# Kernel tuning notes

Hardware: AMD Instinct MI355X
Metric: run time of the kernel (lower is better)

Reference implementation:

```python
import jax, jax.numpy as jnp
import numpy as np

USER_NUM, ITEM_NUM, FACTOR = 138493, 26744, 64
BATCH, N_COLS = 8192, 67  # 1 user + 2 positives + 64 negatives


def setup_inputs() -> dict:
    key = jax.random.key(0)
    k1, k2, k3 = jax.random.split(key, 3)
    one_batch = jax.random.randint(k1, (BATCH, N_COLS), 0, ITEM_NUM, dtype=jnp.int64 if jax.config.jax_enable_x64 else jnp.int32)
    embed_user = jax.random.normal(k2, (USER_NUM, FACTOR), dtype=jnp.float32) * 0.01
    embed_item = jax.random.normal(k3, (ITEM_NUM, FACTOR), dtype=jnp.float32) * 0.01
    return {"one_batch": one_batch, "embed_user": embed_user, "embed_item": embed_item}


def reference(one_batch, embed_user, embed_item):
    user_batch = one_batch[:, 0]          # [B]
    item_batch = one_batch[:, 1:]         # [B, 2+Nneg]
    user_i = embed_user[user_batch]       # [B, D]
    item_i = embed_item[item_batch]       # [B, 2+Nneg, D]

    # scores for the two positives
    z_ai = jnp.einsum('bd,bd->b', user_i, item_i[:, 0, :])
    z_aj = jnp.einsum('bd,bd->b', user_i, item_i[:, 1, :])

    # fun_z with flag=True: |z_ai - z_aj| clamped at 0.5 (pos_sim2 is computed
    # in the original but unused and identical to pos_sim1 by symmetry)
    d = jnp.abs(z_ai - z_aj)
    pos_sim1 = jnp.where(d > 0.5, 0.5, d)

    # all negative scores at once (vectorizes the original Python loop)
    z_ak = jnp.einsum('bd,bnd->bn', user_i, item_i[:, 2:, :])  # [B, Nneg]
    # fun_z with flag=False: -log(sigmoid(z_pos - z_neg))
    neg_sim1 = -jax.nn.log_sigmoid(z_ai[:, None] - z_ak)       # [B, Nneg]
    neg_sim2 = -jax.nn.log_sigmoid(z_aj[:, None] - z_ak)
    one_pn = neg_sim1 + neg_sim2                                # [B, Nneg]

    loss_m6 = one_pn.sum(axis=1)        # running sum over negatives
    loss_m6_min = one_pn.max(axis=1)    # 'min' in the source is actually a running max

    loss_posdis = -jnp.mean(jax.nn.log_sigmoid(pos_sim1 * 2.0 - loss_m6_min))
    loss_pre = loss_posdis + loss_m6.mean()

    l2_regulization = 0.01 * ((user_i ** 2 + (item_i ** 2).sum(axis=1)).sum(axis=-1)).mean()
    loss = loss_pre + l2_regulization
    return (loss, l2_regulization)
```

## Files before the change

### kernel.cpp

```cpp
#include <hip/hip_runtime.h>
#include <math.h>

#define BATCH   8192
#define NCOLS   67
#define DFAC    64
#define THREADS 256
#define WPB     4
#define NBLOCKS (BATCH / WPB)

__device__ __forceinline__ float softplus_f(float t) {
    return fmaxf(t, 0.f) + log1pf(expf(-fabsf(t)));
}
__device__ __forceinline__ float logsig_f(float x) { return -softplus_f(-x); }

__device__ __forceinline__ float wave_sum(float v) {
    #pragma unroll
    for (int off = 32; off; off >>= 1) v += __shfl_xor(v, off);
    return v;
}
__device__ __forceinline__ float wave_max(float v) {
    #pragma unroll
    for (int off = 32; off; off >>= 1) v = fmaxf(v, __shfl_xor(v, off));
    return v;
}

__global__ __launch_bounds__(THREADS) void bpr_main(
    const int*   __restrict__ one_batch,
    const float* __restrict__ eu,
    const float* __restrict__ ei,
    float*       __restrict__ partials)
{
    const int lane = threadIdx.x & 63;
    const int wave = threadIdx.x >> 6;
    const int r    = blockIdx.x * WPB + wave;

    const int rl = lane & 3;
    const int rg = lane >> 2;

    __shared__ float zbuf[WPB][68];

    const int* idx = one_batch + r * NCOLS;

    const int myidx  = idx[lane];
    const int myidx2 = idx[64 + (lane < 3 ? lane : 2)];

    const int uidx = __builtin_amdgcn_readfirstlane(myidx);

    float4 u4[4];
    #pragma unroll
    for (int j = 0; j < 4; ++j)
        u4[j] = *(const float4*)(eu + (size_t)uidx * DFAC + j * 16 + rl * 4);

    float usq = 0.f;
    #pragma unroll
    for (int j = 0; j < 4; ++j)
        usq += u4[j].x*u4[j].x + u4[j].y*u4[j].y + u4[j].z*u4[j].z + u4[j].w*u4[j].w;

    float acc_sq = 0.f;

    #pragma unroll
    for (int s = 0; s < 5; ++s) {
        const int  rr    = s * 16 + rg;
        const bool valid = (rr < 66);
        int col = 1 + rr;
        if (col > 66) col = 66;
        const int ridx = (col < 64) ? __shfl(myidx, col)
                                    : __shfl(myidx2, col - 64);

        const float* vrow = ei + (size_t)ridx * DFAC + rl * 4;
        float pd = 0.f, sq = 0.f;
        #pragma unroll
        for (int j = 0; j < 4; ++j) {
            const float4 v4 = *(const float4*)(vrow + j * 16);
            pd += v4.x*u4[j].x + v4.y*u4[j].y + v4.z*u4[j].z + v4.w*u4[j].w;
            sq += v4.x*v4.x + v4.y*v4.y + v4.z*v4.z + v4.w*v4.w;
        }
        if (valid) acc_sq += sq;

        pd += __shfl_xor(pd, 1);
        pd += __shfl_xor(pd, 2);
        if (valid && rl == 0) zbuf[wave][col] = pd;
    }

    const float z_ai = zbuf[wave][1];
    const float z_aj = zbuf[wave][2];
    const float zak  = zbuf[wave][3 + lane];

    const float one_pn = softplus_f(zak - z_ai) + softplus_f(zak - z_aj);

    const float m6max = wave_max(one_pn);

    float acc_pos = 0.f;
    if (lane == 0) {
        const float dd  = fabsf(z_ai - z_aj);
        const float pos = fminf(dd, 0.5f);
        acc_pos = logsig_f(pos * 2.f - m6max);
    }

    const float acc_m6 = wave_sum(one_pn);
    const float acc_l2 = wave_sum(acc_sq + usq * 0.0625f);

    __shared__ float red[WPB][3];
    if (lane == 0) {
        red[wave][0] = acc_pos;
        red[wave][1] = acc_m6;
        red[wave][2] = acc_l2;
    }
    __syncthreads();
    if (threadIdx.x == 0) {
        float p = 0.f, m = 0.f, l = 0.f;
        #pragma unroll
        for (int w = 0; w < WPB; ++w) {
            p += red[w][0]; m += red[w][1]; l += red[w][2];
        }
        partials[blockIdx.x * 3 + 0] = p;
        partials[blockIdx.x * 3 + 1] = m;
        partials[blockIdx.x * 3 + 2] = l;
    }
}

__global__ __launch_bounds__(256) void bpr_finalize(
    const float* __restrict__ partials, float* __restrict__ out)
{
    float p = 0.f, m = 0.f, l = 0.f;
    for (int i = threadIdx.x; i < NBLOCKS; i += 256) {
        p += partials[i * 3 + 0];
        m += partials[i * 3 + 1];
        l += partials[i * 3 + 2];
    }
    p = wave_sum(p); m = wave_sum(m); l = wave_sum(l);

    __shared__ float red[4][3];
    const int lane = threadIdx.x & 63, wave = threadIdx.x >> 6;
    if (lane == 0) { red[wave][0] = p; red[wave][1] = m; red[wave][2] = l; }
    __syncthreads();
    if (threadIdx.x == 0) {
        #pragma unroll
        for (int w = 1; w < 4; ++w) { p += red[w][0]; m += red[w][1]; l += red[w][2]; }
        const float inv = 1.f / (float)BATCH;
        const float l2   = 0.01f * l * inv;
        const float loss = (-p * inv) + m * inv + l2;
        out[0] = loss;
        out[1] = l2;
    }
}

extern "C" void kernel_launch(void* const* d_in, const int* in_sizes, int n_in,
                              void* d_out, int out_size, void* d_ws, size_t ws_size,
                              hipStream_t stream) {
    const int*   one_batch = (const int*)d_in[0];
    const float* eu        = (const float*)d_in[1];
    const float* ei        = (const float*)d_in[2];
    float* out = (float*)d_out;
    float* partials = (float*)d_ws;

    bpr_main<<<NBLOCKS, THREADS, 0, stream>>>(one_batch, eu, ei, partials);
    bpr_finalize<<<1, 256, 0, stream>>>(partials, out);
}
```

Baseline: 23.55 us.

## Convert item embeddings to bf16 in workspace before gather-dot kernel

Adds a pre-pass kernel that converts the whole item embedding table to bf16 in the workspace on every call. The main kernel then gathers half-size rows, with each lane owning 16 contiguous elements, to cut gather bandwidth. An fp32 fallback path is kept for when the workspace is too small, and invalid rows now skip their loads. The conversion reads and writes the full table (about 6.8 MB) every call, which may cost more than the gather saves, and bf16 rounding reduces accuracy.

```diff
diff --git a/kernel.cpp b/kernel.cpp
--- a/kernel.cpp
+++ b/kernel.cpp
@@ -4,10 +4,15 @@
 #define BATCH   8192
 #define NCOLS   67
 #define DFAC    64
+#define ITEMS   26744
 #define THREADS 256
 #define WPB     4
 #define NBLOCKS (BATCH / WPB)
 
+#define PARTIALS_OFF   0
+#define ITEMBF16_OFF   32768
+#define WS_NEEDED      (ITEMBF16_OFF + (size_t)ITEMS * DFAC * 2)
+
 __device__ __forceinline__ float softplus_f(float t) {
     return fmaxf(t, 0.f) + log1pf(expf(-fabsf(t)));
 }
@@ -24,11 +29,32 @@
     return v;
 }
 
-__global__ __launch_bounds__(THREADS) void bpr_main(
-    const int*   __restrict__ one_batch,
-    const float* __restrict__ eu,
-    const float* __restrict__ ei,
-    float*       __restrict__ partials)
+__device__ __forceinline__ unsigned bf16rne(float f) {
+    unsigned u = __float_as_uint(f);
+    return (u + 0x7FFFu + ((u >> 16) & 1u)) >> 16;
+}
+
+__global__ __launch_bounds__(256) void cvt_items(
+    const float* __restrict__ ei, unsigned* __restrict__ out )
+{
+    const int t = blockIdx.x * 256 + threadIdx.x;
+    const int n8 = ITEMS * DFAC / 8;
+    if (t >= n8) return;
+    const float4 a = *(const float4*)(ei + (size_t)t * 8);
+    const float4 b = *(const float4*)(ei + (size_t)t * 8 + 4);
+    uint4 o;
+    o.x = bf16rne(a.x) | (bf16rne(a.y) << 16);
+    o.y = bf16rne(a.z) | (bf16rne(a.w) << 16);
+    o.z = bf16rne(b.x) | (bf16rne(b.y) << 16);
+    o.w = bf16rne(b.z) | (bf16rne(b.w) << 16);
+    *(uint4*)(out + (size_t)t * 4) = o;
+}
+
+__global__ __launch_bounds__(THREADS) void bpr_main_bf16(
+    const int*      __restrict__ one_batch,
+    const float*    __restrict__ eu,
+    const unsigned* __restrict__ eib,
+    float*          __restrict__ partials)
 {
     const int lane = threadIdx.x & 63;
     const int wave = threadIdx.x >> 6;
@@ -40,16 +66,14 @@
     __shared__ float zbuf[WPB][68];
 
     const int* idx = one_batch + r * NCOLS;
-
     const int myidx  = idx[lane];
     const int myidx2 = idx[64 + (lane < 3 ? lane : 2)];
-
     const int uidx = __builtin_amdgcn_readfirstlane(myidx);
 
     float4 u4[4];
     #pragma unroll
     for (int j = 0; j < 4; ++j)
-        u4[j] = *(const float4*)(eu + (size_t)uidx * DFAC + j * 16 + rl * 4);
+        u4[j] = *(const float4*)(eu + (size_t)uidx * DFAC + rl * 16 + j * 4);
 
     float usq = 0.f;
     #pragma unroll
@@ -62,20 +86,26 @@
     for (int s = 0; s < 5; ++s) {
         const int  rr    = s * 16 + rg;
         const bool valid = (rr < 66);
-        int col = 1 + rr;
-        if (col > 66) col = 66;
+        const int col = valid ? 1 + rr : 66;
         const int ridx = (col < 64) ? __shfl(myidx, col)
                                     : __shfl(myidx2, col - 64);
 
-        const float* vrow = ei + (size_t)ridx * DFAC + rl * 4;
         float pd = 0.f, sq = 0.f;
-        #pragma unroll
-        for (int j = 0; j < 4; ++j) {
-            const float4 v4 = *(const float4*)(vrow + j * 16);
-            pd += v4.x*u4[j].x + v4.y*u4[j].y + v4.z*u4[j].z + v4.w*u4[j].w;
-            sq += v4.x*v4.x + v4.y*v4.y + v4.z*v4.z + v4.w*v4.w;
+        if (valid) {
+            const unsigned* vp = eib + (size_t)ridx * (DFAC / 2) + rl * 8;
+            const uint4 w0 = *(const uint4*)(vp);
+            const uint4 w1 = *(const uint4*)(vp + 4);
+            const unsigned wds[8] = {w0.x, w0.y, w0.z, w0.w, w1.x, w1.y, w1.z, w1.w};
+            const float* uf = (const float*)u4;
+            #pragma unroll
+            for (int e = 0; e < 8; ++e) {
+                const float v0 = __uint_as_float(wds[e] << 16);
+                const float v1 = __uint_as_float(wds[e] & 0xFFFF0000u);
+                pd += v0 * uf[e * 2] + v1 * uf[e * 2 + 1];
+                sq += v0 * v0 + v1 * v1;
+            }
+            acc_sq += sq;
         }
-        if (valid) acc_sq += sq;
 
         pd += __shfl_xor(pd, 1);
         pd += __shfl_xor(pd, 2);
@@ -87,7 +117,6 @@
     const float zak  = zbuf[wave][3 + lane];
 
     const float one_pn = softplus_f(zak - z_ai) + softplus_f(zak - z_aj);
-
     const float m6max = wave_max(one_pn);
 
     float acc_pos = 0.f;
@@ -102,17 +131,91 @@
 
     __shared__ float red[WPB][3];
     if (lane == 0) {
-        red[wave][0] = acc_pos;
-        red[wave][1] = acc_m6;
-        red[wave][2] = acc_l2;
+        red[wave][0] = acc_pos; red[wave][1] = acc_m6; red[wave][2] = acc_l2;
     }
     __syncthreads();
     if (threadIdx.x == 0) {
         float p = 0.f, m = 0.f, l = 0.f;
         #pragma unroll
-        for (int w = 0; w < WPB; ++w) {
-            p += red[w][0]; m += red[w][1]; l += red[w][2];
+        for (int w = 0; w < WPB; ++w) { p += red[w][0]; m += red[w][1]; l += red[w][2]; }
+        partials[blockIdx.x * 3 + 0] = p;
+        partials[blockIdx.x * 3 + 1] = m;
+        partials[blockIdx.x * 3 + 2] = l;
+    }
+}
+
+__global__ __launch_bounds__(THREADS) void bpr_main_f32(
+    const int*   __restrict__ one_batch,
+    const float* __restrict__ eu,
+    const float* __restrict__ ei,
+    float*       __restrict__ partials)
+{
+    const int lane = threadIdx.x & 63;
+    const int wave = threadIdx.x >> 6;
+    const int r    = blockIdx.x * WPB + wave;
+    const int rl = lane & 3;
+    const int rg = lane >> 2;
+
+    __shared__ float zbuf[WPB][68];
+    const int* idx = one_batch + r * NCOLS;
+    const int myidx  = idx[lane];
+    const int myidx2 = idx[64 + (lane < 3 ? lane : 2)];
+    const int uidx = __builtin_amdgcn_readfirstlane(myidx);
+
+    float4 u4[4];
+    #pragma unroll
+    for (int j = 0; j < 4; ++j)
+        u4[j] = *(const float4*)(eu + (size_t)uidx * DFAC + j * 16 + rl * 4);
+    float usq = 0.f;
+    #pragma unroll
+    for (int j = 0; j < 4; ++j)
+        usq += u4[j].x*u4[j].x + u4[j].y*u4[j].y + u4[j].z*u4[j].z + u4[j].w*u4[j].w;
+
+    float acc_sq = 0.f;
+    #pragma unroll
+    for (int s = 0; s < 5; ++s) {
+        const int  rr    = s * 16 + rg;
+        const bool valid = (rr < 66);
+        const int col = valid ? 1 + rr : 66;
+        const int ridx = (col < 64) ? __shfl(myidx, col)
+                                    : __shfl(myidx2, col - 64);
+        float pd = 0.f;
+        if (valid) {
+            const float* vrow = ei + (size_t)ridx * DFAC + rl * 4;
+            float sq = 0.f;
+            #pragma unroll
+            for (int j = 0; j < 4; ++j) {
+                const float4 v4 = *(const float4*)(vrow + j * 16);
+                pd += v4.x*u4[j].x + v4.y*u4[j].y + v4.z*u4[j].z + v4.w*u4[j].w;
+                sq += v4.x*v4.x + v4.y*v4.y + v4.z*v4.z + v4.w*v4.w;
+            }
+            acc_sq += sq;
         }
+        pd += __shfl_xor(pd, 1);
+        pd += __shfl_xor(pd, 2);
+        if (valid && rl == 0) zbuf[wave][col] = pd;
+    }
+
+    const float z_ai = zbuf[wave][1];
+    const float z_aj = zbuf[wave][2];
+    const float zak  = zbuf[wave][3 + lane];
+    const float one_pn = softplus_f(zak - z_ai) + softplus_f(zak - z_aj);
+    const float m6max = wave_max(one_pn);
+    float acc_pos = 0.f;
+    if (lane == 0) {
+        const float dd  = fabsf(z_ai - z_aj);
+        acc_pos = logsig_f(fminf(dd, 0.5f) * 2.f - m6max);
+    }
+    const float acc_m6 = wave_sum(one_pn);
+    const float acc_l2 = wave_sum(acc_sq + usq * 0.0625f);
+
+    __shared__ float red[WPB][3];
+    if (lane == 0) { red[wave][0] = acc_pos; red[wave][1] = acc_m6; red[wave][2] = acc_l2; }
+    __syncthreads();
+    if (threadIdx.x == 0) {
+        float p = 0.f, m = 0.f, l = 0.f;
+        #pragma unroll
+        for (int w = 0; w < WPB; ++w) { p += red[w][0]; m += red[w][1]; l += red[w][2]; }
         partials[blockIdx.x * 3 + 0] = p;
         partials[blockIdx.x * 3 + 1] = m;
         partials[blockIdx.x * 3 + 2] = l;
@@ -152,8 +255,15 @@
     const float* eu        = (const float*)d_in[1];
     const float* ei        = (const float*)d_in[2];
     float* out = (float*)d_out;
-    float* partials = (float*)d_ws;
-
-    bpr_main<<<NBLOCKS, THREADS, 0, stream>>>(one_batch, eu, ei, partials);
+    float* partials = (float*)((char*)d_ws + PARTIALS_OFF);
+
+    if (ws_size >= WS_NEEDED) {
+        unsigned* eib = (unsigned*)((char*)d_ws + ITEMBF16_OFF);
+        const int n8 = ITEMS * DFAC / 8;
+        cvt_items<<<(n8 + 255) / 256, 256, 0, stream>>>(ei, eib);
+        bpr_main_bf16<<<NBLOCKS, THREADS, 0, stream>>>(one_batch, eu, eib, partials);
+    } else {
+        bpr_main_f32<<<NBLOCKS, THREADS, 0, stream>>>(one_batch, eu, ei, partials);
+    }
     bpr_finalize<<<1, 256, 0, stream>>>(partials, out);
 }
```

New measurement: 28.59 us. 21.4% more time.

## Fuse finalize into main kernel via last-block atomic counter, widen lane chunks

Applied to the files above, without the earlier changes.

Merges the separate finalize kernel into the main kernel: each block writes its partials and bumps a global counter, and the last block to arrive performs the final reduction. Each lane now handles 8 floats of a row instead of 4 and stages the indices in shared memory, so the row loop runs in 9 steps instead of 5. A hipMemsetAsync still resets the counter every call, which adds a memset operation while removing the second kernel launch. The goal is to cut launch and tail overhead, at the cost of atomics and fences plus a serialized last-block reduction.

```diff
diff --git a/kernel.cpp b/kernel.cpp
--- a/kernel.cpp
+++ b/kernel.cpp
@@ -7,6 +7,9 @@
 #define THREADS 256
 #define WPB     4
 #define NBLOCKS (BATCH / WPB)
+
+#define COUNTER_OFF   0
+#define PARTIALS_OFF  256
 
 __device__ __forceinline__ float softplus_f(float t) {
     return fmaxf(t, 0.f) + log1pf(expf(-fabsf(t)));
@@ -24,62 +27,65 @@
     return v;
 }
 
-__global__ __launch_bounds__(THREADS) void bpr_main(
+__global__ __launch_bounds__(THREADS) void bpr_fused(
     const int*   __restrict__ one_batch,
     const float* __restrict__ eu,
     const float* __restrict__ ei,
-    float*       __restrict__ partials)
+    float*       __restrict__ partials,
+    unsigned*    __restrict__ counter,
+    float*       __restrict__ out)
 {
     const int lane = threadIdx.x & 63;
     const int wave = threadIdx.x >> 6;
     const int r    = blockIdx.x * WPB + wave;
 
-    const int rl = lane & 3;
-    const int rg = lane >> 2;
+    const int hl  = lane & 7;
+    const int rg8 = lane >> 3;
 
     __shared__ float zbuf[WPB][68];
+    __shared__ int   ibuf[WPB][68];
 
     const int* idx = one_batch + r * NCOLS;
+    ibuf[wave][lane] = idx[lane];
+    if (lane < 3) ibuf[wave][64 + lane] = idx[64 + lane];
 
-    const int myidx  = idx[lane];
-    const int myidx2 = idx[64 + (lane < 3 ? lane : 2)];
+    const int uidx = __builtin_amdgcn_readfirstlane(ibuf[wave][0]);
 
-    const int uidx = __builtin_amdgcn_readfirstlane(myidx);
-
-    float4 u4[4];
-    #pragma unroll
-    for (int j = 0; j < 4; ++j)
-        u4[j] = *(const float4*)(eu + (size_t)uidx * DFAC + j * 16 + rl * 4);
+    const float4 ua = *(const float4*)(eu + (size_t)uidx * DFAC + hl * 8);
+    const float4 ub = *(const float4*)(eu + (size_t)uidx * DFAC + hl * 8 + 4);
+    const float uf[8] = {ua.x, ua.y, ua.z, ua.w, ub.x, ub.y, ub.z, ub.w};
 
     float usq = 0.f;
     #pragma unroll
-    for (int j = 0; j < 4; ++j)
-        usq += u4[j].x*u4[j].x + u4[j].y*u4[j].y + u4[j].z*u4[j].z + u4[j].w*u4[j].w;
+    for (int e = 0; e < 8; ++e) usq += uf[e] * uf[e];
 
     float acc_sq = 0.f;
 
     #pragma unroll
-    for (int s = 0; s < 5; ++s) {
-        const int  rr    = s * 16 + rg;
+    for (int s = 0; s < 9; ++s) {
+        const int  rr    = s * 8 + rg8;
         const bool valid = (rr < 66);
-        int col = 1 + rr;
-        if (col > 66) col = 66;
-        const int ridx = (col < 64) ? __shfl(myidx, col)
-                                    : __shfl(myidx2, col - 64);
+        const int  col   = valid ? 1 + rr : 66;
+        const int  ridx  = ibuf[wave][col];
 
-        const float* vrow = ei + (size_t)ridx * DFAC + rl * 4;
-        float pd = 0.f, sq = 0.f;
-        #pragma unroll
-        for (int j = 0; j < 4; ++j) {
-            const float4 v4 = *(const float4*)(vrow + j * 16);
-            pd += v4.x*u4[j].x + v4.y*u4[j].y + v4.z*u4[j].z + v4.w*u4[j].w;
-            sq += v4.x*v4.x + v4.y*v4.y + v4.z*v4.z + v4.w*v4.w;
+        float pd = 0.f;
+        if (valid) {
+            const float* vrow = ei + (size_t)ridx * DFAC + hl * 8;
+            const float4 va = *(const float4*)(vrow);
+            const float4 vb = *(const float4*)(vrow + 4);
+            const float vf[8] = {va.x, va.y, va.z, va.w, vb.x, vb.y, vb.z, vb.w};
+            float sq = 0.f;
+            #pragma unroll
+            for (int e = 0; e < 8; ++e) {
+                pd += vf[e] * uf[e];
+                sq += vf[e] * vf[e];
+            }
+            acc_sq += sq;
         }
-        if (valid) acc_sq += sq;
-
         pd += __shfl_xor(pd, 1);
         pd += __shfl_xor(pd, 2);
-        if (valid && rl == 0) zbuf[wave][col] = pd;
+        pd += __shfl_xor(pd, 4);
+        if (valid && hl == 0) zbuf[wave][col] = pd;
     }
 
     const float z_ai = zbuf[wave][1];
@@ -87,61 +93,64 @@
     const float zak  = zbuf[wave][3 + lane];
 
     const float one_pn = softplus_f(zak - z_ai) + softplus_f(zak - z_aj);
-
     const float m6max = wave_max(one_pn);
 
     float acc_pos = 0.f;
     if (lane == 0) {
-        const float dd  = fabsf(z_ai - z_aj);
-        const float pos = fminf(dd, 0.5f);
-        acc_pos = logsig_f(pos * 2.f - m6max);
+        const float dd = fabsf(z_ai - z_aj);
+        acc_pos = logsig_f(fminf(dd, 0.5f) * 2.f - m6max);
     }
 
     const float acc_m6 = wave_sum(one_pn);
-    const float acc_l2 = wave_sum(acc_sq + usq * 0.0625f);
+    const float acc_l2 = wave_sum(acc_sq + usq * 0.125f);
 
     __shared__ float red[WPB][3];
+    __shared__ int   isLast;
     if (lane == 0) {
-        red[wave][0] = acc_pos;
-        red[wave][1] = acc_m6;
-        red[wave][2] = acc_l2;
+        red[wave][0] = acc_pos; red[wave][1] = acc_m6; red[wave][2] = acc_l2;
     }
     __syncthreads();
+
     if (threadIdx.x == 0) {
         float p = 0.f, m = 0.f, l = 0.f;
         #pragma unroll
-        for (int w = 0; w < WPB; ++w) {
-            p += red[w][0]; m += red[w][1]; l += red[w][2];
-        }
-        partials[blockIdx.x * 3 + 0] = p;
-        partials[blockIdx.x * 3 + 1] = m;
-        partials[blockIdx.x * 3 + 2] = l;
+        for (int w = 0; w < WPB; ++w) { p += red[w][0]; m += red[w][1]; l += red[w][2]; }
+        __hip_atomic_store(&partials[blockIdx.x],               p,
+                           __ATOMIC_RELAXED, __HIP_MEMORY_SCOPE_AGENT);
+        __hip_atomic_store(&partials[NBLOCKS + blockIdx.x],     m,
+                           __ATOMIC_RELAXED, __HIP_MEMORY_SCOPE_AGENT);
+        __hip_atomic_store(&partials[2 * NBLOCKS + blockIdx.x], l,
+                           __ATOMIC_RELAXED, __HIP_MEMORY_SCOPE_AGENT);
+        __threadfence();
+        const unsigned prev = __hip_atomic_fetch_add(
+            counter, 1u, __ATOMIC_ACQ_REL, __HIP_MEMORY_SCOPE_AGENT);
+        isLast = (prev == NBLOCKS - 1);
     }
-}
+    __syncthreads();
+    if (!isLast) return;
 
-__global__ __launch_bounds__(256) void bpr_finalize(
-    const float* __restrict__ partials, float* __restrict__ out)
-{
+    __threadfence();
     float p = 0.f, m = 0.f, l = 0.f;
-    for (int i = threadIdx.x; i < NBLOCKS; i += 256) {
-        p += partials[i * 3 + 0];
-        m += partials[i * 3 + 1];
-        l += partials[i * 3 + 2];
+    #pragma unroll
+    for (int j = 0; j < NBLOCKS / THREADS; ++j) {
+        const int i = j * THREADS + threadIdx.x;
+        p += __hip_atomic_load(&partials[i],               __ATOMIC_RELAXED, __HIP_MEMORY_SCOPE_AGENT);
+        m += __hip_atomic_load(&partials[NBLOCKS + i],     __ATOMIC_RELAXED, __HIP_MEMORY_SCOPE_AGENT);
+        l += __hip_atomic_load(&partials[2 * NBLOCKS + i], __ATOMIC_RELAXED, __HIP_MEMORY_SCOPE_AGENT);
     }
     p = wave_sum(p); m = wave_sum(m); l = wave_sum(l);
 
-    __shared__ float red[4][3];
-    const int lane = threadIdx.x & 63, wave = threadIdx.x >> 6;
     if (lane == 0) { red[wave][0] = p; red[wave][1] = m; red[wave][2] = l; }
     __syncthreads();
     if (threadIdx.x == 0) {
         #pragma unroll
-        for (int w = 1; w < 4; ++w) { p += red[w][0]; m += red[w][1]; l += red[w][2]; }
-        const float inv = 1.f / (float)BATCH;
+        for (int w = 1; w < WPB; ++w) { p += red[w][0]; m += red[w][1]; l += red[w][2]; }
+        const float inv  = 1.f / (float)BATCH;
         const float l2   = 0.01f * l * inv;
         const float loss = (-p * inv) + m * inv + l2;
         out[0] = loss;
         out[1] = l2;
+        __hip_atomic_store(counter, 0u, __ATOMIC_RELAXED, __HIP_MEMORY_SCOPE_AGENT);
     }
 }
 
@@ -151,9 +160,11 @@
     const int*   one_batch = (const int*)d_in[0];
     const float* eu        = (const float*)d_in[1];
     const float* ei        = (const float*)d_in[2];
-    float* out = (float*)d_out;
-    float* partials = (float*)d_ws;
+    float*    out      = (float*)d_out;
+    unsigned* counter  = (unsigned*)((char*)d_ws + COUNTER_OFF);
+    float*    partials = (float*)((char*)d_ws + PARTIALS_OFF);
 
-    bpr_main<<<NBLOCKS, THREADS, 0, stream>>>(one_batch, eu, ei, partials);
-    bpr_finalize<<<1, 256, 0, stream>>>(partials, out);
+    hipMemsetAsync(counter, 0, sizeof(unsigned), stream);
+    bpr_fused<<<NBLOCKS, THREADS, 0, stream>>>(one_batch, eu, ei,
+                                               partials, counter, out);
 }
```

Measured after the change: 84.25 us. 3.58x slower.
